# Performance work log

Measured on AMD Instinct MI355X. Metric: run time of the kernel, lower is better.

Reference implementation:

```python
import jax, jax.numpy as jnp
import numpy as np

B, BS, WS = 2, 1024, 512
D_IN, H, DH, DFF = 2048, 16, 128, 8192
DM = H * DH


def _ln(x, g, eps=1e-5):
    m = x.mean(-1, keepdims=True)
    v = ((x - m) ** 2).mean(-1, keepdims=True)
    return (x - m) / jnp.sqrt(v + eps) * g


def _rotate_half(x):
    p = x.reshape(x.shape[:-1] + (-1, 2))
    a, b = p[..., 0], p[..., 1]
    return jnp.stack([-b, a], axis=-1).reshape(x.shape)


def _rope(x, freqs, scale):
    # xpos convention: align rotary table from the end for shorter sequences
    f = freqs[-x.shape[1]:]
    s = scale[-x.shape[1]:]
    return x * jnp.cos(f) * s + _rotate_half(x) * jnp.sin(f) * s


def setup_inputs():
    key = jax.random.key(0)
    ks = jax.random.split(key, 12)
    def w(k, shape, s=0.02):
        return jax.random.normal(k, shape, dtype=jnp.float32) * s
    x = jax.random.normal(ks[0], (B, BS, D_IN), dtype=jnp.float32)
    cache_k = jnp.zeros((B, WS, DM), jnp.float32)  # first call: zero KV cache
    cache_v = jnp.zeros((B, WS, DM), jnp.float32)
    # rotary frequencies over concatenated length, interleaved pairs
    pos = jnp.arange(BS + WS, dtype=jnp.float32)
    inv = 1.0 / (10000.0 ** (jnp.arange(0, DM, 2, dtype=jnp.float32) / DM))
    rotary = jnp.repeat(pos[:, None] * inv[None, :], 2, axis=-1)  # [BS+WS, DM]
    xscale = jax.random.uniform(ks[1], (BS + WS, DM), jnp.float32, 0.8, 1.2)
    # sliding window mask: query i (abs pos WS+i) sees keys j with i < j <= i+WS
    i = np.arange(BS)[:, None]
    j = np.arange(BS + WS)[None, :]
    mask = jnp.asarray(((j > i) & (j <= i + WS)).astype(np.int32))
    return dict(
        x=x, cache_k=cache_k, cache_v=cache_v, rotary=rotary, xscale=xscale, mask=mask,
        g_in=jnp.ones((D_IN,), jnp.float32),
        Wq=w(ks[2], (DM, D_IN)), Wk=w(ks[3], (DM, D_IN)), Wv=w(ks[4], (DM, D_IN)),
        g_q=jnp.ones((DM,), jnp.float32), g_k=jnp.ones((DM,), jnp.float32),
        Wlq=w(ks[5], (DM, DM)), blq=jnp.zeros((DM,), jnp.float32),
        Wlk=w(ks[6], (DM, DM)), blk=jnp.zeros((DM,), jnp.float32),
        Wlv=w(ks[7], (DM, DM)), blv=jnp.zeros((DM,), jnp.float32),
        Wo=w(ks[8], (DM, DM)), bo=jnp.zeros((DM,), jnp.float32),
        g_ffn=jnp.ones((DM,), jnp.float32),
        W1=w(ks[9], (DFF, DM)), W2=w(ks[10], (D_IN, DFF)))


def reference(x, cache_k, cache_v, rotary, xscale, mask, g_in, Wq, Wk, Wv, g_q, g_k,
              Wlq, blq, Wlk, blk, Wlv, blv, Wo, bo, g_ffn, W1, W2):
    xn = _ln(x, g_in)
    q = _ln(xn @ Wq.T, g_q)            # [B, BS, DM]
    k = _ln(xn @ Wk.T, g_k)
    v = xn @ Wv.T
    k = jnp.concatenate([cache_k, k], axis=1)  # [B, WS+BS, DM]
    v = jnp.concatenate([cache_v, v], axis=1)
    q_r = _rope(q, rotary, xscale)
    k_r = _rope(k, rotary, 1.0 / xscale)
    def heads(t):
        return t.reshape(t.shape[0], -1, H, DH).transpose(0, 2, 1, 3)
    qh = heads(q_r @ Wlq.T + blq)      # [B, H, BS, DH]
    kh = heads(k_r @ Wlk.T + blk)      # [B, H, WS+BS, DH]
    vh = heads(v @ Wlv.T + blv)
    scores = jnp.einsum('bhqd,bhkd->bhqk', qh, kh) / jnp.float32(np.sqrt(DH))
    scores = jnp.where(mask == 0, jnp.float32(-1e9), scores)
    p = jax.nn.softmax(scores, axis=-1)
    o = jnp.einsum('bhqk,bhkd->bhqd', p, vh)
    o = o.transpose(0, 2, 1, 3).reshape(x.shape[0], -1, DM) @ Wo.T + bo
    return jax.nn.relu(_ln(o, g_ffn) @ W1.T) @ W2.T
```

## Files before the change

kernel.cpp:

```cpp
#include <hip/hip_runtime.h>

typedef unsigned short u16;
typedef __attribute__((ext_vector_type(8))) __bf16 bf16x8;
typedef __attribute__((ext_vector_type(4))) float f32x4;

__device__ __forceinline__ float b2f(u16 u) {
    unsigned int i = ((unsigned int)u) << 16;
    return __builtin_bit_cast(float, i);
}
__device__ __forceinline__ u16 f2b(float f) {
    unsigned int x = __builtin_bit_cast(unsigned int, f);
    x += 0x7fffu + ((x >> 16) & 1u);
    return (u16)(x >> 16);
}
__device__ __forceinline__ void gld_lds16(const void* g, void* l) {
    __builtin_amdgcn_global_load_lds(
        (const __attribute__((address_space(1))) unsigned int*)g,
        (__attribute__((address_space(3))) unsigned int*)l, 16, 0, 0);
}

__global__ __launch_bounds__(256) void cvt_f32_bf16(
    const float* __restrict__ in, u16* __restrict__ out, int n4)
{
    int i = blockIdx.x * 256 + threadIdx.x;
    if (i < n4) {
        float4 v = ((const float4*)in)[i];
        ushort4 o;
        o.x = f2b(v.x); o.y = f2b(v.y); o.z = f2b(v.z); o.w = f2b(v.w);
        ((ushort4*)out)[i] = o;
    }
}

__global__ __launch_bounds__(256) void zero_f32(float* __restrict__ p, int n4)
{
    int i = blockIdx.x * 256 + threadIdx.x;
    if (i < n4) ((float4*)p)[i] = (float4){0.f, 0.f, 0.f, 0.f};
}

enum { EP_BF16 = 0, EP_BF16_BIAS, EP_BF16_RELU, EP_BF16_KV, EP_BF16_BIAS_VT, EP_F32_OUT };

template <int MODE>
__global__ __launch_bounds__(256) void gemm_bt(
    const u16* __restrict__ A, const u16* __restrict__ W,
    const float* __restrict__ bias, void* __restrict__ out,
    int M, int N, int K)
{
    __shared__ u16 As[128 * 64];
    __shared__ u16 Bs[128 * 64];
    const int tid = threadIdx.x;
    const int row0 = blockIdx.y * 128, col0 = blockIdx.x * 128;
    const int wave = tid >> 6, lane = tid & 63, quad = lane >> 4, l16 = lane & 15;
    const int wm = (wave >> 1) * 64, wn = (wave & 1) * 64;

    f32x4 acc[4][4];
#pragma unroll
    for (int i = 0; i < 4; ++i)
#pragma unroll
        for (int j = 0; j < 4; ++j) acc[i][j] = (f32x4){0.f, 0.f, 0.f, 0.f};

    const char* Ab = (const char*)A + (size_t)row0 * K * 2;
    const char* Wb = (const char*)W + (size_t)col0 * K * 2;
    const size_t ldb = (size_t)K * 2;

    for (int k0 = 0; k0 < K; k0 += 64) {
#pragma unroll
        for (int r = 0; r < 4; ++r) {
            int o = r * 4096 + tid * 16;
            int trow = o >> 7, tcolb = o & 127;
            gld_lds16(Ab + (size_t)trow * ldb + (size_t)k0 * 2 + tcolb, (char*)As + o);
            gld_lds16(Wb + (size_t)trow * ldb + (size_t)k0 * 2 + tcolb, (char*)Bs + o);
        }
        __syncthreads();
#pragma unroll
        for (int ks = 0; ks < 2; ++ks) {
            bf16x8 af[4], bfr[4];
#pragma unroll
            for (int i = 0; i < 4; ++i)
                af[i] = *(const bf16x8*)(As + (wm + i * 16 + l16) * 64 + ks * 32 + quad * 8);
#pragma unroll
            for (int j = 0; j < 4; ++j)
                bfr[j] = *(const bf16x8*)(Bs + (wn + j * 16 + l16) * 64 + ks * 32 + quad * 8);
#pragma unroll
            for (int i = 0; i < 4; ++i)
#pragma unroll
                for (int j = 0; j < 4; ++j)
                    acc[i][j] = __builtin_amdgcn_mfma_f32_16x16x32_bf16(af[i], bfr[j], acc[i][j], 0, 0, 0);
        }
        __syncthreads();
    }

#pragma unroll
    for (int j = 0; j < 4; ++j) {
        int gcol = col0 + wn + j * 16 + l16;
        float bv = 0.f;
        if (MODE == EP_BF16_BIAS || MODE == EP_BF16_BIAS_VT) bv = bias[gcol];
#pragma unroll
        for (int i = 0; i < 4; ++i) {
            int growb = row0 + wm + i * 16 + quad * 4;
#pragma unroll
            for (int reg = 0; reg < 4; ++reg) {
                int grow = growb + reg;
                float v = acc[i][j][reg] + bv;
                if (MODE == EP_BF16_RELU) v = fmaxf(v, 0.f);
                if (MODE == EP_F32_OUT) {
                    ((float*)out)[(size_t)grow * N + gcol] = v;
                } else if (MODE == EP_BF16_KV) {
                    int b = grow >> 10, s = grow & 1023;
                    ((u16*)out)[((size_t)(b * 1536 + 512 + s)) * N + gcol] = f2b(v);
                } else if (MODE == EP_BF16_BIAS_VT) {
                    int b = (grow >= 1536) ? 1 : 0;
                    int jk = grow - b * 1536;
                    ((u16*)out)[((size_t)(b * 2048 + gcol)) * 1536 + jk] = f2b(v);
                } else {
                    ((u16*)out)[(size_t)grow * N + gcol] = f2b(v);
                }
            }
        }
    }
}

struct FuseA { const u16* A; const u16* W; const float* bias; void* out; int M; int mode; };
struct Fuse3 { FuseA z0, z1, z2; };

__global__ __launch_bounds__(256) void gemm_bt_f(Fuse3 f, int K)
{
    FuseA p = (blockIdx.z == 0) ? f.z0 : ((blockIdx.z == 1) ? f.z1 : f.z2);
    const int row0 = blockIdx.y * 128, col0 = blockIdx.x * 128;
    if (row0 >= p.M) return;

    __shared__ u16 As[128 * 64];
    __shared__ u16 Bs[128 * 64];
    const int tid = threadIdx.x;
    const int wave = tid >> 6, lane = tid & 63, quad = lane >> 4, l16 = lane & 15;
    const int wm = (wave >> 1) * 64, wn = (wave & 1) * 64;

    f32x4 acc[4][4];
#pragma unroll
    for (int i = 0; i < 4; ++i)
#pragma unroll
        for (int j = 0; j < 4; ++j) acc[i][j] = (f32x4){0.f, 0.f, 0.f, 0.f};

    const char* Ab = (const char*)p.A + (size_t)row0 * K * 2;
    const char* Wb = (const char*)p.W + (size_t)col0 * K * 2;
    const size_t ldb = (size_t)K * 2;

    for (int k0 = 0; k0 < K; k0 += 64) {
#pragma unroll
        for (int r = 0; r < 4; ++r) {
            int o = r * 4096 + tid * 16;
            int trow = o >> 7, tcolb = o & 127;
            gld_lds16(Ab + (size_t)trow * ldb + (size_t)k0 * 2 + tcolb, (char*)As + o);
            gld_lds16(Wb + (size_t)trow * ldb + (size_t)k0 * 2 + tcolb, (char*)Bs + o);
        }
        __syncthreads();
#pragma unroll
        for (int ks = 0; ks < 2; ++ks) {
            bf16x8 af[4], bfr[4];
#pragma unroll
            for (int i = 0; i < 4; ++i)
                af[i] = *(const bf16x8*)(As + (wm + i * 16 + l16) * 64 + ks * 32 + quad * 8);
#pragma unroll
            for (int j = 0; j < 4; ++j)
                bfr[j] = *(const bf16x8*)(Bs + (wn + j * 16 + l16) * 64 + ks * 32 + quad * 8);
#pragma unroll
            for (int i = 0; i < 4; ++i)
#pragma unroll
                for (int j = 0; j < 4; ++j)
                    acc[i][j] = __builtin_amdgcn_mfma_f32_16x16x32_bf16(af[i], bfr[j], acc[i][j], 0, 0, 0);
        }
        __syncthreads();
    }

#pragma unroll
    for (int j = 0; j < 4; ++j) {
        int gcol = col0 + wn + j * 16 + l16;
        float bv = (p.mode == EP_BF16_BIAS || p.mode == EP_BF16_BIAS_VT) ? p.bias[gcol] : 0.f;
#pragma unroll
        for (int i = 0; i < 4; ++i) {
            int growb = row0 + wm + i * 16 + quad * 4;
#pragma unroll
            for (int reg = 0; reg < 4; ++reg) {
                int grow = growb + reg;
                u16 hv = f2b(acc[i][j][reg] + bv);
                size_t idx;
                if (p.mode == EP_BF16_KV) {
                    int b = grow >> 10, s = grow & 1023;
                    idx = ((size_t)(b * 1536 + 512 + s)) * 2048 + gcol;
                } else if (p.mode == EP_BF16_BIAS_VT) {
                    int b = (grow >= 1536) ? 1 : 0;
                    int jk = grow - b * 1536;
                    idx = ((size_t)(b * 2048 + gcol)) * 1536 + jk;
                } else {
                    idx = (size_t)grow * 2048 + gcol;
                }
                ((u16*)p.out)[idx] = hv;
            }
        }
    }
}

__global__ __launch_bounds__(256) void gemm_bt_sk(
    const u16* __restrict__ A, const u16* __restrict__ W,
    const float* __restrict__ bias, float* __restrict__ out,
    int N, int K, int Kc)
{
    __shared__ u16 As[128 * 64];
    __shared__ u16 Bs[128 * 64];
    const int tid = threadIdx.x;
    const int row0 = blockIdx.y * 128, col0 = blockIdx.x * 128;
    const int wave = tid >> 6, lane = tid & 63, quad = lane >> 4, l16 = lane & 15;
    const int wm = (wave >> 1) * 64, wn = (wave & 1) * 64;
    const int kbeg = blockIdx.z * Kc, kend = kbeg + Kc;

    f32x4 acc[4][4];
#pragma unroll
    for (int i = 0; i < 4; ++i)
#pragma unroll
        for (int j = 0; j < 4; ++j) acc[i][j] = (f32x4){0.f, 0.f, 0.f, 0.f};

    const char* Ab = (const char*)A + (size_t)row0 * K * 2;
    const char* Wb = (const char*)W + (size_t)col0 * K * 2;
    const size_t ldb = (size_t)K * 2;

    for (int k0 = kbeg; k0 < kend; k0 += 64) {
#pragma unroll
        for (int r = 0; r < 4; ++r) {
            int o = r * 4096 + tid * 16;
            int trow = o >> 7, tcolb = o & 127;
            gld_lds16(Ab + (size_t)trow * ldb + (size_t)k0 * 2 + tcolb, (char*)As + o);
            gld_lds16(Wb + (size_t)trow * ldb + (size_t)k0 * 2 + tcolb, (char*)Bs + o);
        }
        __syncthreads();
#pragma unroll
        for (int ks = 0; ks < 2; ++ks) {
            bf16x8 af[4], bfr[4];
#pragma unroll
            for (int i = 0; i < 4; ++i)
                af[i] = *(const bf16x8*)(As + (wm + i * 16 + l16) * 64 + ks * 32 + quad * 8);
#pragma unroll
            for (int j = 0; j < 4; ++j)
                bfr[j] = *(const bf16x8*)(Bs + (wn + j * 16 + l16) * 64 + ks * 32 + quad * 8);
#pragma unroll
            for (int i = 0; i < 4; ++i)
#pragma unroll
                for (int j = 0; j < 4; ++j)
                    acc[i][j] = __builtin_amdgcn_mfma_f32_16x16x32_bf16(af[i], bfr[j], acc[i][j], 0, 0, 0);
        }
        __syncthreads();
    }

#pragma unroll
    for (int j = 0; j < 4; ++j) {
        int gcol = col0 + wn + j * 16 + l16;
        float bv = (bias != nullptr && blockIdx.z == 0) ? bias[gcol] : 0.f;
#pragma unroll
        for (int i = 0; i < 4; ++i) {
            int growb = row0 + wm + i * 16 + quad * 4;
#pragma unroll
            for (int reg = 0; reg < 4; ++reg) {
                int grow = growb + reg;
                atomicAdd(&out[(size_t)grow * N + gcol], acc[i][j][reg] + bv);
            }
        }
    }
}

template <int IN_F32>
__global__ __launch_bounds__(256) void ln_rows(
    const void* __restrict__ in, const float* __restrict__ gamma,
    u16* __restrict__ out)
{
    const int row = blockIdx.x, tid = threadIdx.x;
    const float* inf = (const float*)in + (size_t)row * 2048;
    const u16* inb = (const u16*)in + (size_t)row * 2048;
    float v[8], s1 = 0.f, s2 = 0.f;
#pragma unroll
    for (int i = 0; i < 8; ++i) {
        int c = tid + i * 256;
        float x = IN_F32 ? inf[c] : b2f(inb[c]);
        v[i] = x; s1 += x; s2 += x * x;
    }
#pragma unroll
    for (int off = 32; off >= 1; off >>= 1) { s1 += __shfl_xor(s1, off, 64); s2 += __shfl_xor(s2, off, 64); }
    __shared__ float ra[4], rb[4];
    int wave = tid >> 6, lane = tid & 63;
    if (lane == 0) { ra[wave] = s1; rb[wave] = s2; }
    __syncthreads();
    s1 = ra[0] + ra[1] + ra[2] + ra[3];
    s2 = rb[0] + rb[1] + rb[2] + rb[3];
    float mean = s1 * (1.f / 2048.f);
    float var = s2 * (1.f / 2048.f) - mean * mean;
    float rstd = rsqrtf(var + 1e-5f);
#pragma unroll
    for (int i = 0; i < 8; ++i) {
        int c = tid + i * 256;
        out[(size_t)row * 2048 + c] = f2b((v[i] - mean) * rstd * gamma[c]);
    }
}

__global__ __launch_bounds__(256) void qk_post(
    const u16* __restrict__ qpre, const u16* __restrict__ kpre,
    const float* __restrict__ gq, const float* __restrict__ gk,
    const float* __restrict__ rotary, const float* __restrict__ xscale,
    u16* __restrict__ qrope, u16* __restrict__ kfull)
{
    const int is_k = blockIdx.x & 1;
    const int row = blockIdx.x >> 1;
    const int b = row >> 10, s = row & 1023;
    const int tid = threadIdx.x, base = tid * 8;
    const u16* in = (is_k ? kpre : qpre) + (size_t)row * 2048;
    float v[8], s1 = 0.f, s2 = 0.f;
#pragma unroll
    for (int i = 0; i < 8; ++i) { float x = b2f(in[base + i]); v[i] = x; s1 += x; s2 += x * x; }
#pragma unroll
    for (int off = 32; off >= 1; off >>= 1) { s1 += __shfl_xor(s1, off, 64); s2 += __shfl_xor(s2, off, 64); }
    __shared__ float ra[4], rb[4];
    int wave = tid >> 6, lane = tid & 63;
    if (lane == 0) { ra[wave] = s1; rb[wave] = s2; }
    __syncthreads();
    s1 = ra[0] + ra[1] + ra[2] + ra[3];
    s2 = rb[0] + rb[1] + rb[2] + rb[3];
    float mean = s1 * (1.f / 2048.f);
    float rstd = rsqrtf(s2 * (1.f / 2048.f) - mean * mean + 1e-5f);
    const float* g = is_k ? gk : gq;
    const int rr = 512 + s;
    u16* outp = is_k ? (kfull + ((size_t)(b * 1536 + 512 + s)) * 2048)
                     : (qrope + (size_t)row * 2048);
#pragma unroll
    for (int p = 0; p < 4; ++p) {
        int e0 = base + 2 * p, e1 = e0 + 1;
        float x0 = (v[2 * p] - mean) * rstd * g[e0];
        float x1 = (v[2 * p + 1] - mean) * rstd * g[e1];
        float f = rotary[(size_t)rr * 2048 + e0];
        float sn, cs; sincosf(f, &sn, &cs);
        float sc0 = xscale[(size_t)rr * 2048 + e0];
        float sc1 = xscale[(size_t)rr * 2048 + e1];
        if (is_k) { sc0 = 1.f / sc0; sc1 = 1.f / sc1; }
        outp[e0] = f2b((x0 * cs - x1 * sn) * sc0);
        outp[e1] = f2b((x1 * cs + x0 * sn) * sc1);
    }
}

__global__ __launch_bounds__(256) void cache_prep(
    const float* __restrict__ cache_k, const float* __restrict__ cache_v,
    const float* __restrict__ rotary, const float* __restrict__ xscale,
    u16* __restrict__ kfull, u16* __restrict__ vfull)
{
    const int row = blockIdx.x;
    const int b = row >> 9, j = row & 511;
    const int base = threadIdx.x * 8;
    const float* ck = cache_k + ((size_t)row) * 2048;
    const float* cv = cache_v + ((size_t)row) * 2048;
    u16* ko = kfull + ((size_t)(b * 1536 + j)) * 2048;
    u16* vo = vfull + ((size_t)(b * 1536 + j)) * 2048;
#pragma unroll
    for (int p = 0; p < 4; ++p) {
        int e0 = base + 2 * p, e1 = e0 + 1;
        float x0 = ck[e0], x1 = ck[e1];
        float f = rotary[(size_t)j * 2048 + e0];
        float sn, cs; sincosf(f, &sn, &cs);
        float sc0 = 1.f / xscale[(size_t)j * 2048 + e0];
        float sc1 = 1.f / xscale[(size_t)j * 2048 + e1];
        ko[e0] = f2b((x0 * cs - x1 * sn) * sc0);
        ko[e1] = f2b((x1 * cs + x0 * sn) * sc1);
        vo[e0] = f2b(cv[e0]); vo[e1] = f2b(cv[e1]);
    }
}

__global__ __launch_bounds__(256) void attn(
    const u16* __restrict__ qh, const u16* __restrict__ kh,
    const u16* __restrict__ vt, u16* __restrict__ o)
{
    __shared__ u16 Qs[16 * 128];
    __shared__ float Ss[16 * 544];
    __shared__ u16 Ps[16 * 544];
    __shared__ float Ls[16];
    const int qt = blockIdx.x, h = blockIdx.y, b = blockIdx.z;
    const int i0 = qt * 16;
    const int tid = threadIdx.x;
    const int wave = tid >> 6, lane = tid & 63, quad = lane >> 4, l16 = lane & 15;

    {
        int r = tid >> 4, seg = tid & 15;
        const u16* src = qh + ((size_t)(b * 1024 + i0 + r)) * 2048 + h * 128 + seg * 8;
        *(uint4*)(Qs + r * 128 + seg * 8) = *(const uint4*)src;
    }
    __syncthreads();

    const float sm = 0.08838834764831845f;
    for (int kt = wave; kt < 33; kt += 4) {
        int jb = i0 + kt * 16;
        const u16* krow = kh + ((size_t)(b * 1536 + jb + l16)) * 2048 + h * 128 + quad * 8;
        const u16* qrow = Qs + l16 * 128 + quad * 8;
        f32x4 sacc = (f32x4){0.f, 0.f, 0.f, 0.f};
#pragma unroll
        for (int st = 0; st < 4; ++st) {
            bf16x8 aq = *(const bf16x8*)(qrow + st * 32);
            bf16x8 bk = *(const bf16x8*)(krow + st * 32);
            sacc = __builtin_amdgcn_mfma_f32_16x16x32_bf16(aq, bk, sacc, 0, 0, 0);
        }
        int jj = jb + l16;
#pragma unroll
        for (int reg = 0; reg < 4; ++reg) {
            int qi = i0 + quad * 4 + reg;
            bool valid = (jj > qi) && (jj <= qi + 512);
            Ss[(quad * 4 + reg) * 544 + kt * 16 + l16] = valid ? sacc[reg] * sm : -1e9f;
        }
    }
    __syncthreads();

    {
        int g = tid >> 4, l = tid & 15;
        float m = -1e30f;
        for (int j = l; j < 528; j += 16) m = fmaxf(m, Ss[g * 544 + j]);
#pragma unroll
        for (int off = 8; off >= 1; off >>= 1) m = fmaxf(m, __shfl_xor(m, off, 16));
        float sum = 0.f;
        for (int j = l; j < 528; j += 16) {
            float e = __expf(Ss[g * 544 + j] - m);
            sum += e;
            Ps[g * 544 + j] = f2b(e);
        }
        Ps[g * 544 + 528 + l] = 0;
#pragma unroll
        for (int off = 8; off >= 1; off >>= 1) sum += __shfl_xor(sum, off, 16);
        if (l == 0) Ls[g] = sum;
    }
    __syncthreads();

    f32x4 oa0 = (f32x4){0.f, 0.f, 0.f, 0.f}, oa1 = oa0;
    const u16* vbase = vt + ((size_t)(b * 2048 + h * 128 + wave * 32 + l16)) * 1536 + i0;
    for (int jc = 0; jc < 17; ++jc) {
        bf16x8 pf = *(const bf16x8*)(Ps + l16 * 544 + jc * 32 + quad * 8);
        bf16x8 v0 = *(const bf16x8*)(vbase + jc * 32 + quad * 8);
        bf16x8 v1 = *(const bf16x8*)(vbase + (size_t)16 * 1536 + jc * 32 + quad * 8);
        oa0 = __builtin_amdgcn_mfma_f32_16x16x32_bf16(pf, v0, oa0, 0, 0, 0);
        oa1 = __builtin_amdgcn_mfma_f32_16x16x32_bf16(pf, v1, oa1, 0, 0, 0);
    }
#pragma unroll
    for (int reg = 0; reg < 4; ++reg) {
        int q = quad * 4 + reg;
        float inv = 1.f / Ls[q];
        size_t orow = ((size_t)(b * 1024 + i0 + q)) * 2048 + h * 128 + wave * 32;
        o[orow + l16] = f2b(oa0[reg] * inv);
        o[orow + 16 + l16] = f2b(oa1[reg] * inv);
    }
}

extern "C" void kernel_launch(void* const* d_in, const int* in_sizes, int n_in,
                              void* d_out, int out_size, void* d_ws, size_t ws_size,
                              hipStream_t stream)
{
    const float* x       = (const float*)d_in[0];
    const float* cache_k = (const float*)d_in[1];
    const float* cache_v = (const float*)d_in[2];
    const float* rotary  = (const float*)d_in[3];
    const float* xscale  = (const float*)d_in[4];
    const float* g_in = (const float*)d_in[6];
    const float* Wq   = (const float*)d_in[7];
    const float* Wk   = (const float*)d_in[8];
    const float* Wv   = (const float*)d_in[9];
    const float* g_q  = (const float*)d_in[10];
    const float* g_k  = (const float*)d_in[11];
    const float* Wlq  = (const float*)d_in[12];
    const float* blq  = (const float*)d_in[13];
    const float* Wlk  = (const float*)d_in[14];
    const float* blk  = (const float*)d_in[15];
    const float* Wlv  = (const float*)d_in[16];
    const float* blv  = (const float*)d_in[17];
    const float* Wo   = (const float*)d_in[18];
    const float* bo   = (const float*)d_in[19];
    const float* g_ffn= (const float*)d_in[20];
    const float* W1   = (const float*)d_in[21];
    const float* W2   = (const float*)d_in[22];

    char* ws = (char*)d_ws;
    u16* xn     = (u16*)(ws + 0);
    u16* qpre   = (u16*)(ws + 8388608);
    u16* kpre   = (u16*)(ws + 16777216);
    u16* wq_b   = (u16*)(ws + 25165824);
    u16* khb    = (u16*)(ws + 25165824);
    u16* vfull  = (u16*)(ws + 37748736);
    u16* wv_b   = (u16*)(ws + 50331648);
    u16* kfull  = (u16*)(ws + 50331648);
    u16* wk_b   = (u16*)(ws + 62914560);
    u16* vt     = (u16*)(ws + 62914560);
    u16* qrope  = (u16*)(ws + 75563008);
    u16* wlq_b  = (u16*)(ws + 83951616);
    u16* wlk_b  = (u16*)(ws + 92340224);
    u16* wlv_b  = (u16*)(ws + 100728832);
    u16* h2     = (u16*)(ws + 83951616);
    u16* qhb    = qpre;
    u16* obuf   = xn;
    u16* h1     = qrope;
    float* opre32 = (float*)(ws + 8388608);
    u16* wo_b   = (u16*)(ws + 25165824);
    u16* w1_b   = (u16*)(ws + 37748736);
    u16* w2_b   = (u16*)(ws + 37748736);

    const int N4M = 4194304 / 4;
    const int N16M = 16777216 / 4;
    const int NZ4M = 4194304 / 4;

    ln_rows<1><<<2048, 256, 0, stream>>>(x, g_in, xn);
    cvt_f32_bf16<<<N4M / 256, 256, 0, stream>>>(Wq, wq_b, N4M);
    cvt_f32_bf16<<<N4M / 256, 256, 0, stream>>>(Wk, wk_b, N4M);
    cvt_f32_bf16<<<N4M / 256, 256, 0, stream>>>(Wv, wv_b, N4M);

    Fuse3 fq;
    fq.z0 = FuseA{xn, wq_b, nullptr, (void*)qpre,  2048, EP_BF16};
    fq.z1 = FuseA{xn, wk_b, nullptr, (void*)kpre,  2048, EP_BF16};
    fq.z2 = FuseA{xn, wv_b, nullptr, (void*)vfull, 2048, EP_BF16_KV};
    gemm_bt_f<<<dim3(16, 16, 3), 256, 0, stream>>>(fq, 2048);

    cache_prep<<<1024, 256, 0, stream>>>(cache_k, cache_v, rotary, xscale, kfull, vfull);
    qk_post<<<4096, 256, 0, stream>>>(qpre, kpre, g_q, g_k, rotary, xscale, qrope, kfull);
    cvt_f32_bf16<<<N4M / 256, 256, 0, stream>>>(Wlq, wlq_b, N4M);
    cvt_f32_bf16<<<N4M / 256, 256, 0, stream>>>(Wlk, wlk_b, N4M);
    cvt_f32_bf16<<<N4M / 256, 256, 0, stream>>>(Wlv, wlv_b, N4M);

    Fuse3 fl;
    fl.z0 = FuseA{qrope, wlq_b, blq, (void*)qhb, 2048, EP_BF16_BIAS};
    fl.z1 = FuseA{kfull, wlk_b, blk, (void*)khb, 3072, EP_BF16_BIAS};
    fl.z2 = FuseA{vfull, wlv_b, blv, (void*)vt,  3072, EP_BF16_BIAS_VT};
    gemm_bt_f<<<dim3(16, 24, 3), 256, 0, stream>>>(fl, 2048);

    attn<<<dim3(64, 16, 2), 256, 0, stream>>>(qhb, khb, vt, obuf);

    cvt_f32_bf16<<<N4M / 256, 256, 0, stream>>>(Wo, wo_b, N4M);
    zero_f32<<<NZ4M / 256, 256, 0, stream>>>(opre32, NZ4M);
    gemm_bt_sk<<<dim3(16, 16, 2), 256, 0, stream>>>(obuf, wo_b, bo, opre32, 2048, 2048, 1024);
    ln_rows<1><<<2048, 256, 0, stream>>>(opre32, g_ffn, h1);

    cvt_f32_bf16<<<N16M / 256, 256, 0, stream>>>(W1, w1_b, N16M);
    gemm_bt<EP_BF16_RELU><<<dim3(64, 16), 256, 0, stream>>>(h1, w1_b, nullptr, h2, 2048, 8192, 2048);
    cvt_f32_bf16<<<N16M / 256, 256, 0, stream>>>(W2, w2_b, N16M);

    zero_f32<<<NZ4M / 256, 256, 0, stream>>>((float*)d_out, NZ4M);
    gemm_bt_sk<<<dim3(16, 16, 4), 256, 0, stream>>>(h2, w2_b, nullptr, (float*)d_out, 2048, 8192, 2048);
}
```

Baseline: 947.3 us.

## Replace atomic split-K with partial buffers reduced in LN and a reduce kernel

Split-K GEMMs now write plain stores into separate per-slice fp32 partial buffers instead of atomicAdd into a zeroed output. The Wo projection uses four K slices whose partials are summed inside a new LN kernel. The W2 GEMM writes three partials plus the output and a reduce kernel adds them. Weight conversions of Q/K/V and Lq/Lk/Lv are batched into single launches. Together these remove the zeroing kernels and atomic contention, at the cost of extra partial-buffer traffic and workspace aliasing.

```diff
diff --git a/kernel.cpp b/kernel.cpp
--- a/kernel.cpp
+++ b/kernel.cpp
@@ -19,22 +19,35 @@
         (__attribute__((address_space(3))) unsigned int*)l, 16, 0, 0);
 }
 
-__global__ __launch_bounds__(256) void cvt_f32_bf16(
-    const float* __restrict__ in, u16* __restrict__ out, int n4)
-{
+struct CVT3 { const float* s0; u16* d0; const float* s1; u16* d1;
+              const float* s2; u16* d2; };
+__global__ __launch_bounds__(256) void cvt3_f32_bf16(CVT3 c, int n4)
+{
+    const float* s = (blockIdx.z == 0) ? c.s0 : ((blockIdx.z == 1) ? c.s1 : c.s2);
+    u16* d = (blockIdx.z == 0) ? c.d0 : ((blockIdx.z == 1) ? c.d1 : c.d2);
     int i = blockIdx.x * 256 + threadIdx.x;
     if (i < n4) {
-        float4 v = ((const float4*)in)[i];
+        float4 v = ((const float4*)s)[i];
         ushort4 o;
         o.x = f2b(v.x); o.y = f2b(v.y); o.z = f2b(v.z); o.w = f2b(v.w);
-        ((ushort4*)out)[i] = o;
-    }
-}
-
-__global__ __launch_bounds__(256) void zero_f32(float* __restrict__ p, int n4)
+        ((ushort4*)d)[i] = o;
+    }
+}
+
+__global__ __launch_bounds__(256) void reduce3_into(
+    const float* __restrict__ p0, const float* __restrict__ p1,
+    const float* __restrict__ p2, float* __restrict__ io, int n4)
 {
     int i = blockIdx.x * 256 + threadIdx.x;
-    if (i < n4) ((float4*)p)[i] = (float4){0.f, 0.f, 0.f, 0.f};
+    if (i < n4) {
+        float4 a = ((const float4*)p0)[i];
+        float4 b = ((const float4*)p1)[i];
+        float4 c = ((const float4*)p2)[i];
+        float4 d = ((float4*)io)[i];
+        d.x += a.x + b.x + c.x; d.y += a.y + b.y + c.y;
+        d.z += a.z + b.z + c.z; d.w += a.w + b.w + c.w;
+        ((float4*)io)[i] = d;
+    }
 }
 
 enum { EP_BF16 = 0, EP_BF16_BIAS, EP_BF16_RELU, EP_BF16_KV, EP_BF16_BIAS_VT, EP_F32_OUT };
@@ -199,10 +212,10 @@
     }
 }
 
-__global__ __launch_bounds__(256) void gemm_bt_sk(
-    const u16* __restrict__ A, const u16* __restrict__ W,
-    const float* __restrict__ bias, float* __restrict__ out,
-    int N, int K, int Kc)
+struct SKP { const u16* A; const u16* W; const float* bias;
+             float* o0; float* o1; float* o2; float* o3; int N, K, Kc; };
+
+__global__ __launch_bounds__(256) void gemm_bt_p(SKP s)
 {
     __shared__ u16 As[128 * 64];
     __shared__ u16 Bs[128 * 64];
@@ -210,7 +223,9 @@
     const int row0 = blockIdx.y * 128, col0 = blockIdx.x * 128;
     const int wave = tid >> 6, lane = tid & 63, quad = lane >> 4, l16 = lane & 15;
     const int wm = (wave >> 1) * 64, wn = (wave & 1) * 64;
-    const int kbeg = blockIdx.z * Kc, kend = kbeg + Kc;
+    const int z = blockIdx.z;
+    float* out = (z == 0) ? s.o0 : ((z == 1) ? s.o1 : ((z == 2) ? s.o2 : s.o3));
+    const int kbeg = z * s.Kc, kend = kbeg + s.Kc;
 
     f32x4 acc[4][4];
 #pragma unroll
@@ -218,9 +233,9 @@
 #pragma unroll
         for (int j = 0; j < 4; ++j) acc[i][j] = (f32x4){0.f, 0.f, 0.f, 0.f};
 
-    const char* Ab = (const char*)A + (size_t)row0 * K * 2;
-    const char* Wb = (const char*)W + (size_t)col0 * K * 2;
-    const size_t ldb = (size_t)K * 2;
+    const char* Ab = (const char*)s.A + (size_t)row0 * s.K * 2;
+    const char* Wb = (const char*)s.W + (size_t)col0 * s.K * 2;
+    const size_t ldb = (size_t)s.K * 2;
 
     for (int k0 = kbeg; k0 < kend; k0 += 64) {
 #pragma unroll
@@ -252,14 +267,14 @@
 #pragma unroll
     for (int j = 0; j < 4; ++j) {
         int gcol = col0 + wn + j * 16 + l16;
-        float bv = (bias != nullptr && blockIdx.z == 0) ? bias[gcol] : 0.f;
+        float bv = (s.bias != nullptr && z == 0) ? s.bias[gcol] : 0.f;
 #pragma unroll
         for (int i = 0; i < 4; ++i) {
             int growb = row0 + wm + i * 16 + quad * 4;
 #pragma unroll
             for (int reg = 0; reg < 4; ++reg) {
                 int grow = growb + reg;
-                atomicAdd(&out[(size_t)grow * N + gcol], acc[i][j][reg] + bv);
+                out[(size_t)grow * s.N + gcol] = acc[i][j][reg] + bv;
             }
         }
     }
@@ -295,6 +310,37 @@
     for (int i = 0; i < 8; ++i) {
         int c = tid + i * 256;
         out[(size_t)row * 2048 + c] = f2b((v[i] - mean) * rstd * gamma[c]);
+    }
+}
+
+__global__ __launch_bounds__(256) void ln4_rows(
+    const float* __restrict__ p0, const float* __restrict__ p1,
+    const float* __restrict__ p2, const float* __restrict__ p3,
+    const float* __restrict__ gamma, u16* __restrict__ out)
+{
+    const int row = blockIdx.x, tid = threadIdx.x;
+    const size_t rb_ = (size_t)row * 2048;
+    float v[8], s1 = 0.f, s2 = 0.f;
+#pragma unroll
+    for (int i = 0; i < 8; ++i) {
+        int c = tid + i * 256;
+        float x = p0[rb_ + c] + p1[rb_ + c] + p2[rb_ + c] + p3[rb_ + c];
+        v[i] = x; s1 += x; s2 += x * x;
+    }
+#pragma unroll
+    for (int off = 32; off >= 1; off >>= 1) { s1 += __shfl_xor(s1, off, 64); s2 += __shfl_xor(s2, off, 64); }
+    __shared__ float ra[4], rbs[4];
+    int wave = tid >> 6, lane = tid & 63;
+    if (lane == 0) { ra[wave] = s1; rbs[wave] = s2; }
+    __syncthreads();
+    s1 = ra[0] + ra[1] + ra[2] + ra[3];
+    s2 = rbs[0] + rbs[1] + rbs[2] + rbs[3];
+    float mean = s1 * (1.f / 2048.f);
+    float rstd = rsqrtf(s2 * (1.f / 2048.f) - mean * mean + 1e-5f);
+#pragma unroll
+    for (int i = 0; i < 8; ++i) {
+        int c = tid + i * 256;
+        out[rb_ + c] = f2b((v[i] - mean) * rstd * gamma[c]);
     }
 }
 
@@ -493,19 +539,23 @@
     u16* qhb    = qpre;
     u16* obuf   = xn;
     u16* h1     = qrope;
-    float* opre32 = (float*)(ws + 8388608);
     u16* wo_b   = (u16*)(ws + 25165824);
-    u16* w1_b   = (u16*)(ws + 37748736);
-    u16* w2_b   = (u16*)(ws + 37748736);
-
-    const int N4M = 4194304 / 4;
-    const int N16M = 16777216 / 4;
-    const int NZ4M = 4194304 / 4;
+    u16* w1_b   = (u16*)(ws + 0);
+    u16* w2_b   = (u16*)(ws + 0);
+    float* WP0  = (float*)(ws + 33554432);
+    float* WP1  = (float*)(ws + 50331648);
+    float* WP2  = (float*)(ws + 83951616);
+    float* WP3  = (float*)(ws + 8388608);
+    float* FP0  = (float*)(ws + 33554432);
+    float* FP1  = (float*)(ws + 50331648);
+    float* FP2  = (float*)(ws + 67108864);
+
+    const int N1M = 4194304 / 4;
+    const int N4M = 16777216 / 4;
 
     ln_rows<1><<<2048, 256, 0, stream>>>(x, g_in, xn);
-    cvt_f32_bf16<<<N4M / 256, 256, 0, stream>>>(Wq, wq_b, N4M);
-    cvt_f32_bf16<<<N4M / 256, 256, 0, stream>>>(Wk, wk_b, N4M);
-    cvt_f32_bf16<<<N4M / 256, 256, 0, stream>>>(Wv, wv_b, N4M);
+    cvt3_f32_bf16<<<dim3(N1M / 256, 1, 3), 256, 0, stream>>>(
+        CVT3{Wq, wq_b, Wk, wk_b, Wv, wv_b}, N1M);
 
     Fuse3 fq;
     fq.z0 = FuseA{xn, wq_b, nullptr, (void*)qpre,  2048, EP_BF16};
@@ -515,9 +565,8 @@
 
     cache_prep<<<1024, 256, 0, stream>>>(cache_k, cache_v, rotary, xscale, kfull, vfull);
     qk_post<<<4096, 256, 0, stream>>>(qpre, kpre, g_q, g_k, rotary, xscale, qrope, kfull);
-    cvt_f32_bf16<<<N4M / 256, 256, 0, stream>>>(Wlq, wlq_b, N4M);
-    cvt_f32_bf16<<<N4M / 256, 256, 0, stream>>>(Wlk, wlk_b, N4M);
-    cvt_f32_bf16<<<N4M / 256, 256, 0, stream>>>(Wlv, wlv_b, N4M);
+    cvt3_f32_bf16<<<dim3(N1M / 256, 1, 3), 256, 0, stream>>>(
+        CVT3{Wlq, wlq_b, Wlk, wlk_b, Wlv, wlv_b}, N1M);
 
     Fuse3 fl;
     fl.z0 = FuseA{qrope, wlq_b, blq, (void*)qhb, 2048, EP_BF16_BIAS};
@@ -527,15 +576,19 @@
 
     attn<<<dim3(64, 16, 2), 256, 0, stream>>>(qhb, khb, vt, obuf);
 
-    cvt_f32_bf16<<<N4M / 256, 256, 0, stream>>>(Wo, wo_b, N4M);
-    zero_f32<<<NZ4M / 256, 256, 0, stream>>>(opre32, NZ4M);
-    gemm_bt_sk<<<dim3(16, 16, 2), 256, 0, stream>>>(obuf, wo_b, bo, opre32, 2048, 2048, 1024);
-    ln_rows<1><<<2048, 256, 0, stream>>>(opre32, g_ffn, h1);
-
-    cvt_f32_bf16<<<N16M / 256, 256, 0, stream>>>(W1, w1_b, N16M);
+    cvt3_f32_bf16<<<dim3(N1M / 256, 1, 1), 256, 0, stream>>>(
+        CVT3{Wo, wo_b, Wo, wo_b, Wo, wo_b}, N1M);
+    gemm_bt_p<<<dim3(16, 16, 4), 256, 0, stream>>>(
+        SKP{obuf, wo_b, bo, WP0, WP1, WP2, WP3, 2048, 2048, 512});
+    ln4_rows<<<2048, 256, 0, stream>>>(WP0, WP1, WP2, WP3, g_ffn, h1);
+
+    cvt3_f32_bf16<<<dim3(N4M / 256, 1, 1), 256, 0, stream>>>(
+        CVT3{W1, w1_b, W1, w1_b, W1, w1_b}, N4M);
     gemm_bt<EP_BF16_RELU><<<dim3(64, 16), 256, 0, stream>>>(h1, w1_b, nullptr, h2, 2048, 8192, 2048);
-    cvt_f32_bf16<<<N16M / 256, 256, 0, stream>>>(W2, w2_b, N16M);
-
-    zero_f32<<<NZ4M / 256, 256, 0, stream>>>((float*)d_out, NZ4M);
-    gemm_bt_sk<<<dim3(16, 16, 4), 256, 0, stream>>>(h2, w2_b, nullptr, (float*)d_out, 2048, 8192, 2048);
-}
+
+    cvt3_f32_bf16<<<dim3(N4M / 256, 1, 1), 256, 0, stream>>>(
+        CVT3{W2, w2_b, W2, w2_b, W2, w2_b}, N4M);
+    gemm_bt_p<<<dim3(16, 16, 4), 256, 0, stream>>>(
+        SKP{h2, w2_b, nullptr, FP0, FP1, FP2, (float*)d_out, 2048, 8192, 2048});
+    reduce3_into<<<N1M / 256, 256, 0, stream>>>(FP0, FP1, FP2, (float*)d_out, N1M);
+}
```

Result: faster. 908.9 us (-4.1%).
